# Performance work log

Hardware: AMD Instinct MI355X
Metric: run time of the kernel (lower is better)

## Reference

```python
import jax, jax.numpy as jnp
import numpy as np

ETYPES = ((0, 2), (4, 6))  # per-metapath edge-type indices into the doubled r_vec table
ALPHA = 3.0


def celu3(x):
    return jax.nn.celu(x, alpha=ALPHA)


def cmul(a, b):
    # complex multiply, last dim = (real, imag)
    re = a[..., 0] * b[..., 0] - a[..., 1] * b[..., 1]
    im = a[..., 0] * b[..., 1] + a[..., 1] * b[..., 0]
    return jnp.stack([re, im], axis=-1)


def setup_inputs() -> dict:
    key = jax.random.key(0)
    ks = jax.random.split(key, 10)
    N, H, heads, M, E, P = 50000, 64, 4, 2, 250000, 3
    R, FH = 4, 128
    D = heads * H
    return {
        "features": jax.random.normal(ks[0], (N, H), jnp.float32),
        "r_vec": jax.random.normal(ks[1], (R, H // 2, 2), jnp.float32),
        "attn1_w": jax.random.normal(ks[2], (heads, H), jnp.float32) * 0.1,
        "attn2": jax.random.normal(ks[3], (1, heads, H), jnp.float32) * 0.1,
        "fw1": jax.random.normal(ks[4], (2 * FH, D), jnp.float32) * 0.05,
        "fb1": jnp.zeros((2 * FH,), jnp.float32),
        "fw2": jax.random.normal(ks[5], (FH, 2 * FH), jnp.float32) * 0.05,
        "fb2": jnp.zeros((FH,), jnp.float32),
        "fw3": jax.random.normal(ks[6], (1, FH), jnp.float32) * 0.05,
        "instances": jax.random.randint(ks[7], (M, E, P), 0, N, jnp.int32),
    }


def reference(features, r_vec, attn1_w, attn2, fw1, fb1, fw2, fb2, fw3, instances):
    N, H = features.shape
    M, E, P = instances.shape
    heads = attn1_w.shape[0]
    # unit-modulus rotations + conjugates: [2R, H/2, 2], even=r, odd=conj(r)
    rv = r_vec / jnp.linalg.norm(r_vec, axis=2, keepdims=True)
    conj = rv * jnp.array([1.0, -1.0], rv.dtype)
    rv2 = jnp.stack([rv, conj], axis=1).reshape(-1, H // 2, 2)

    per_path = []
    for m in range(M):
        inst = instances[m]  # [E, P]
        # backward cumulative rotation: final_r[i] = prod_{j>=i} r_{etype[j]}, final_r[P-1]=1
        ident = jnp.stack([jnp.ones(H // 2, rv.dtype), jnp.zeros(H // 2, rv.dtype)], axis=-1)
        frs = [ident]
        for i in range(P - 2, -1, -1):
            frs.insert(0, cmul(frs[0], rv2[ETYPES[m][i]]))
        fr = jnp.stack(frs)  # [P, H/2, 2]
        # gather features along metapath and rotate (last position rotated by identity)
        edata = features[inst].reshape(E, P, H // 2, 2)
        rot = cmul(edata, fr[None])
        me = jnp.mean(rot.reshape(E, P, H), axis=1)  # [E, H]
        se = celu3(me) * jax.nn.sigmoid(me)  # gated metapath embedding
        eft = celu3(se)  # same across heads in original (tiled)
        seg = inst[:, 0]  # target node per instance
        a1 = celu3(features[seg] @ attn1_w.T)  # [E, heads]
        a2 = jnp.einsum('eh,kh->ek', eft, attn2[0])  # [E, heads]
        a = celu3(a1 + a2)
        # segment softmax over each node's instance set
        amax = jax.ops.segment_max(a, seg, num_segments=N)
        ex = jnp.exp(a - amax[seg])
        den = jax.ops.segment_sum(ex, seg, num_segments=N)
        attn = ex / den[seg]  # [E, heads]
        hsum = jax.ops.segment_sum(attn[:, :, None] * eft[:, None, :], seg, num_segments=N)
        per_path.append(celu3(hsum).reshape(N, heads * H))  # empty nodes -> 0

    z = jnp.stack(per_path, axis=1)  # [N, M, D]
    t = celu3(z @ fw1.T + fb1)
    t = celu3(t @ fw2.T + fb2)
    w = (t @ fw3.T).mean(axis=0)  # [M, 1]
    beta = jax.nn.softmax(w, axis=0)
    out = (beta * z).sum(axis=1)  # [N, D]
    return out
```

## Files before the change

kernel.cpp:

```cpp
#include <hip/hip_runtime.h>
#include <hip/hip_bf16.h>

typedef unsigned short u16;
typedef unsigned int   u32;
typedef short bf16x8 __attribute__((ext_vector_type(8)));
typedef float f32x4  __attribute__((ext_vector_type(4)));

#define CAP 64

__device__ inline float b2f(u16 u){ return __builtin_bit_cast(float, (u32)u << 16); }
__device__ inline u16 f2b(float f){
  u32 x = __builtin_bit_cast(u32, f);
  x += 0x7fffu + ((x >> 16) & 1u);
  return (u16)(x >> 16);
}
__device__ inline u32 pk2(float lo, float hi){
  float2 f; f.x = lo; f.y = hi;
  __hip_bfloat162 h = __float22bfloat162_rn(f);
  u32 r; __builtin_memcpy(&r, &h, 4);
  return r;
}
__device__ inline void up2(u32 u, float& lo, float& hi){
  lo = __builtin_bit_cast(float, u << 16);
  hi = __builtin_bit_cast(float, u & 0xffff0000u);
}
__device__ inline float fexp(float x){ return __expf(x); }
__device__ inline float celu3(float x){
  return x > 0.f ? x : 3.f * (__expf(x * (1.f/3.f)) - 1.f);
}
__device__ inline float sigm(float x){ return 1.f / (1.f + __expf(-x)); }

__global__ __launch_bounds__(256) void conv_kernel(
    const float* __restrict__ src, u16* __restrict__ dst, int n8)
{
  int i = blockIdx.x * 256 + threadIdx.x;
  if (i >= n8) return;
  float4 a = ((const float4*)src)[2*i], b = ((const float4*)src)[2*i + 1];
  uint4 o;
  o.x = pk2(a.x, a.y);
  o.y = pk2(a.z, a.w);
  o.z = pk2(b.x, b.y);
  o.w = pk2(b.z, b.w);
  ((uint4*)dst)[i] = o;
}

__global__ __launch_bounds__(256) void a1_kernel(
    const float* __restrict__ feat, const float* __restrict__ attn1,
    u16* __restrict__ featb, float* __restrict__ a1c, int N)
{
  __shared__ float w1s[256];
  int t = threadIdx.x;
  w1s[t] = attn1[t];
  __syncthreads();
  int g = t >> 4, l = t & 15;
  int n = blockIdx.x * 16 + g;
  if (n >= N) return;
  float4 x = ((const float4*)feat)[(size_t)n*16 + l];
  uint2 o;
  o.x = pk2(x.x, x.y);
  o.y = pk2(x.z, x.w);
  ((uint2*)featb)[(size_t)n*16 + l] = o;
  float d[4];
  #pragma unroll
  for (int k = 0; k < 4; ++k){
    int wb = k*64 + l*4;
    d[k] = x.x*w1s[wb] + x.y*w1s[wb+1] + x.z*w1s[wb+2] + x.w*w1s[wb+3];
  }
  #pragma unroll
  for (int off = 8; off; off >>= 1){
    #pragma unroll
    for (int k = 0; k < 4; ++k) d[k] += __shfl_xor(d[k], off);
  }
  if (l == 0){
    float4 av;
    av.x = celu3(d[0]); av.y = celu3(d[1]);
    av.z = celu3(d[2]); av.w = celu3(d[3]);
    ((float4*)a1c)[n] = av;
  }
}

__global__ void fr_kernel(const float* __restrict__ rvec, float* __restrict__ fr){
  int c = threadIdx.x;
  if (c >= 32) return;
  for (int m = 0; m < 2; ++m){
    float ar = rvec[(2*m)*64 + c*2],   ai = rvec[(2*m)*64 + c*2 + 1];
    float br = rvec[(2*m+1)*64 + c*2], bi = rvec[(2*m+1)*64 + c*2 + 1];
    float na = rsqrtf(ar*ar + ai*ai); ar *= na; ai *= na;
    float nb = rsqrtf(br*br + bi*bi); br *= nb; bi *= nb;
    float* f = fr + m*128;
    f[c*2]        = br*ar - bi*ai;
    f[c*2 + 1]    = br*ai + bi*ar;
    f[64 + c*2]   = br;
    f[64 + c*2+1] = bi;
  }
}

__global__ __launch_bounds__(256) void edge_kernel(
    const u16* __restrict__ featb, const int* __restrict__ inst,
    const float* __restrict__ fr, const float* __restrict__ a1c,
    const float* __restrict__ attn2, u16* __restrict__ eft,
    float* __restrict__ a_ws, int* __restrict__ cnt, int* __restrict__ bucket,
    int E, int N)
{
  __shared__ float frs[128];
  __shared__ float w2s[256];
  int m = blockIdx.y;
  int t = threadIdx.x;
  if (t < 128) frs[t] = fr[m*128 + t];
  w2s[t] = attn2[t];
  __syncthreads();

  int g = t >> 4, l = t & 15;
  int e = blockIdx.x * 16 + g;
  if (e >= E) return;
  int base = (m*E + e)*3;
  int i0 = inst[base], i1 = inst[base+1], i2 = inst[base+2];

  const uint2* fb = (const uint2*)featb;
  uint2 v0 = fb[(size_t)i0*16 + l];
  uint2 v1 = fb[(size_t)i1*16 + l];
  uint2 v2 = fb[(size_t)i2*16 + l];
  float f0[4], f1[4], f2v[4];
  up2(v0.x, f0[0], f0[1]); up2(v0.y, f0[2], f0[3]);
  up2(v1.x, f1[0], f1[1]); up2(v1.y, f1[2], f1[3]);
  up2(v2.x, f2v[0], f2v[1]); up2(v2.y, f2v[2], f2v[3]);

  float4 R0 = *(const float4*)&frs[4*l];
  float4 R1 = *(const float4*)&frs[64 + 4*l];

  float mre0 = (f0[0]*R0.x - f0[1]*R0.y + f1[0]*R1.x - f1[1]*R1.y + f2v[0]) * (1.f/3.f);
  float mim0 = (f0[0]*R0.y + f0[1]*R0.x + f1[0]*R1.y + f1[1]*R1.x + f2v[1]) * (1.f/3.f);
  float mre1 = (f0[2]*R0.z - f0[3]*R0.w + f1[2]*R1.z - f1[3]*R1.w + f2v[2]) * (1.f/3.f);
  float mim1 = (f0[2]*R0.w + f0[3]*R0.z + f1[2]*R1.w + f1[3]*R1.z + f2v[3]) * (1.f/3.f);

  float ef[4], s;
  s = celu3(mre0) * sigm(mre0); ef[0] = celu3(s);
  s = celu3(mim0) * sigm(mim0); ef[1] = celu3(s);
  s = celu3(mre1) * sigm(mre1); ef[2] = celu3(s);
  s = celu3(mim1) * sigm(mim1); ef[3] = celu3(s);

  uint2 uo;
  uo.x = pk2(ef[0], ef[1]);
  uo.y = pk2(ef[2], ef[3]);
  ((uint2*)eft)[(size_t)(m*E + e)*16 + l] = uo;

  float d2[4];
  #pragma unroll
  for (int k = 0; k < 4; ++k){
    int wb = k*64 + l*4;
    d2[k] = ef[0]*w2s[wb] + ef[1]*w2s[wb+1] + ef[2]*w2s[wb+2] + ef[3]*w2s[wb+3];
  }
  #pragma unroll
  for (int off = 8; off; off >>= 1){
    #pragma unroll
    for (int k = 0; k < 4; ++k) d2[k] += __shfl_xor(d2[k], off);
  }
  if (l == 0){
    float4 a1v = ((const float4*)a1c)[i0];
    float4 av;
    av.x = celu3(a1v.x + d2[0]);
    av.y = celu3(a1v.y + d2[1]);
    av.z = celu3(a1v.z + d2[2]);
    av.w = celu3(a1v.w + d2[3]);
    ((float4*)a_ws)[m*E + e] = av;
    int pos = atomicAdd(&cnt[m*N + i0], 1);
    if (pos < CAP) bucket[(size_t)(m*N + i0)*CAP + pos] = e;
  }
}

__global__ __launch_bounds__(256) void seg_kernel(
    const float* __restrict__ a_ws, const u16* __restrict__ eft,
    const int* __restrict__ cnt, const int* __restrict__ bucket,
    u16* __restrict__ z, int E, int N)
{
  int m = blockIdx.y;
  int n = blockIdx.x * 4 + (threadIdx.x >> 6);
  if (n >= N) return;
  int lane = threadIdx.x & 63;
  int sidx = m*N + n;
  int deg = cnt[sidx]; if (deg > CAP) deg = CAP;

  float h0=0.f, h1=0.f, h2=0.f, h3=0.f;
  float d0=0.f, d1=0.f, d2=0.f, d3=0.f;
  if (deg > 0){
    const int* bk = bucket + (size_t)sidx * CAP;
    size_t ebase = (size_t)m * E;

    int e = (lane < deg) ? bk[lane] : 0;
    float w0 = 0.f, w1 = 0.f, w2 = 0.f, w3 = 0.f;
    if (lane < deg){
      float4 av = ((const float4*)a_ws)[ebase + e];
      w0 = fexp(av.x); w1 = fexp(av.y); w2 = fexp(av.z); w3 = fexp(av.w);
    }

    const u16* ep = eft + ebase*64;
    for (int j = 0; j < deg; ++j){
      int   ej  = __shfl(e,  j);
      float a0j = __shfl(w0, j), a1j = __shfl(w1, j);
      float a2j = __shfl(w2, j), a3j = __shfl(w3, j);
      float ev = b2f(ep[(size_t)ej*64 + lane]);
      h0 += a0j*ev; h1 += a1j*ev; h2 += a2j*ev; h3 += a3j*ev;
      d0 += a0j;    d1 += a1j;    d2 += a2j;    d3 += a3j;
    }
    h0 /= d0; h1 /= d1; h2 /= d2; h3 /= d3;
  }
  u16* zr = z + (size_t)sidx*256 + lane;
  zr[0]   = f2b(celu3(h0));
  zr[64]  = f2b(celu3(h1));
  zr[128] = f2b(celu3(h2));
  zr[192] = f2b(celu3(h3));
}

__global__ __launch_bounds__(512, 4) void mlp_kernel(
    const u16* __restrict__ z, const u16* __restrict__ fw1b, const float* __restrict__ fb1,
    const u16* __restrict__ fw2b, const float* __restrict__ fb2, const float* __restrict__ fw3,
    float* __restrict__ waccP, int rows, int N)
{
  __shared__ u16 buf[64][264];
  __shared__ float fw3s[128];
  __shared__ float sPart[8][64];
  int tid = threadIdx.x;
  int row0 = blockIdx.x * 64;
  int wv = tid >> 6, lane = tid & 63, lr = lane & 15, quad = lane >> 4;

  const uint4* zg = (const uint4*)z;
  uint4 zr4[4];
  #pragma unroll
  for (int it = 0; it < 4; ++it){
    int idx = it*512 + tid;
    int row = idx >> 5, c8 = idx & 31;
    int gr = row0 + row;
    zr4[it] = make_uint4(0u,0u,0u,0u);
    if (gr < rows) zr4[it] = zg[(size_t)gr*32 + c8];
  }

  const u16* wb1 = fw1b + (size_t)(wv*32 + lr)*256 + quad*8;
  bf16x8 B1[2][8];
  #pragma unroll
  for (int nt = 0; nt < 2; ++nt)
    #pragma unroll
    for (int ks = 0; ks < 8; ++ks)
      B1[nt][ks] = *(const bf16x8*)(wb1 + nt*16*256 + ks*32);

  if (tid < 128) fw3s[tid] = fw3[tid];

  #pragma unroll
  for (int it = 0; it < 4; ++it){
    int idx = it*512 + tid;
    int row = idx >> 5, c8 = idx & 31;
    *(uint4*)&buf[row][c8*8] = zr4[it];
  }
  __syncthreads();

  f32x4 zero4 = {0.f, 0.f, 0.f, 0.f};

  f32x4 acc[4][2];
  #pragma unroll
  for (int a = 0; a < 4; ++a){ acc[a][0] = zero4; acc[a][1] = zero4; }
  #pragma unroll
  for (int ks = 0; ks < 8; ++ks){
    #pragma unroll
    for (int mt = 0; mt < 4; ++mt){
      bf16x8 af = *(const bf16x8*)&buf[mt*16 + lr][ks*32 + quad*8];
      acc[mt][0] = __builtin_amdgcn_mfma_f32_16x16x32_bf16(af, B1[0][ks], acc[mt][0], 0, 0, 0);
      acc[mt][1] = __builtin_amdgcn_mfma_f32_16x16x32_bf16(af, B1[1][ks], acc[mt][1], 0, 0, 0);
    }
  }

  const u16* wb2 = fw2b + (size_t)(wv*16 + lr)*256 + quad*8;
  bf16x8 B2[8];
  #pragma unroll
  for (int ks = 0; ks < 8; ++ks)
    B2[ks] = *(const bf16x8*)(wb2 + ks*32);

  __syncthreads();
  #pragma unroll
  for (int nt = 0; nt < 2; ++nt){
    int col = wv*32 + nt*16 + lr;
    float bias = fb1[col];
    #pragma unroll
    for (int mt = 0; mt < 4; ++mt)
      #pragma unroll
      for (int ri = 0; ri < 4; ++ri){
        int row = mt*16 + quad*4 + ri;
        buf[row][col] = f2b(celu3(acc[mt][nt][ri] + bias));
      }
  }
  __syncthreads();

  f32x4 acc2[4];
  #pragma unroll
  for (int a = 0; a < 4; ++a) acc2[a] = zero4;
  #pragma unroll
  for (int ks = 0; ks < 8; ++ks){
    #pragma unroll
    for (int mt = 0; mt < 4; ++mt){
      bf16x8 af = *(const bf16x8*)&buf[mt*16 + lr][ks*32 + quad*8];
      acc2[mt] = __builtin_amdgcn_mfma_f32_16x16x32_bf16(af, B2[ks], acc2[mt], 0, 0, 0);
    }
  }

  {
    int col = wv*16 + lr;
    float bias2 = fb2[col];
    float w3 = fw3s[col];
    float ps[4][4];
    #pragma unroll
    for (int mt = 0; mt < 4; ++mt)
      #pragma unroll
      for (int ri = 0; ri < 4; ++ri)
        ps[mt][ri] = celu3(acc2[mt][ri] + bias2) * w3;
    #pragma unroll
    for (int off = 8; off; off >>= 1)
      #pragma unroll
      for (int mt = 0; mt < 4; ++mt)
        #pragma unroll
        for (int ri = 0; ri < 4; ++ri)
          ps[mt][ri] += __shfl_xor(ps[mt][ri], off);
    if (lr == 0){
      #pragma unroll
      for (int mt = 0; mt < 4; ++mt)
        #pragma unroll
        for (int ri = 0; ri < 4; ++ri)
          sPart[wv][mt*16 + quad*4 + ri] = ps[mt][ri];
    }
  }
  __syncthreads();

  if (tid < 64){
    float s = 0.f;
    #pragma unroll
    for (int w = 0; w < 8; ++w) s += sPart[w][tid];
    int gr = row0 + tid;
    if (gr >= rows) s = 0.f;
    float s0 = (gr < N) ? s : 0.f;
    float s1 = (gr < N) ? 0.f : s;
    #pragma unroll
    for (int off = 32; off; off >>= 1){
      s0 += __shfl_xor(s0, off);
      s1 += __shfl_xor(s1, off);
    }
    if (tid == 0){
      int slot = blockIdx.x & 63;
      atomicAdd(&waccP[slot],      s0);
      atomicAdd(&waccP[64 + slot], s1);
    }
  }
}

__global__ void beta_kernel(float* __restrict__ wacc, float invN){
  int t = threadIdx.x;
  float s0 = wacc[t], s1 = wacc[64 + t];
  #pragma unroll
  for (int off = 32; off; off >>= 1){
    s0 += __shfl_xor(s0, off);
    s1 += __shfl_xor(s1, off);
  }
  if (t == 0){
    float w0 = s0*invN, w1 = s1*invN;
    float mx = fmaxf(w0, w1);
    float e0 = __expf(w0 - mx), e1 = __expf(w1 - mx);
    float s = e0 + e1;
    wacc[128] = e0 / s;
    wacc[129] = e1 / s;
  }
}

__global__ __launch_bounds__(256) void out_kernel(
    const u16* __restrict__ z, const float* __restrict__ wacc,
    float* __restrict__ out, int total)
{
  int idx = blockIdx.x * 256 + threadIdx.x;
  if (idx*8 >= total) return;
  float b0 = wacc[128], b1 = wacc[129];
  uint4 u0 = ((const uint4*)z)[idx];
  uint4 u1 = ((const uint4*)z)[(total >> 3) + idx];
  float a0,a1v,c0,c1;
  float4 o;
  up2(u0.x, a0, a1v); up2(u1.x, c0, c1);
  o.x = b0*a0 + b1*c0; o.y = b0*a1v + b1*c1;
  up2(u0.y, a0, a1v); up2(u1.y, c0, c1);
  o.z = b0*a0 + b1*c0; o.w = b0*a1v + b1*c1;
  ((float4*)out)[idx*2] = o;
  up2(u0.z, a0, a1v); up2(u1.z, c0, c1);
  o.x = b0*a0 + b1*c0; o.y = b0*a1v + b1*c1;
  up2(u0.w, a0, a1v); up2(u1.w, c0, c1);
  o.z = b0*a0 + b1*c0; o.w = b0*a1v + b1*c1;
  ((float4*)out)[idx*2 + 1] = o;
}

extern "C" void kernel_launch(void* const* d_in, const int* in_sizes, int n_in,
                              void* d_out, int out_size, void* d_ws, size_t ws_size,
                              hipStream_t stream)
{
  (void)n_in; (void)out_size; (void)ws_size;
  const float* feat  = (const float*)d_in[0];
  const float* rvec  = (const float*)d_in[1];
  const float* attn1 = (const float*)d_in[2];
  const float* attn2 = (const float*)d_in[3];
  const float* fw1   = (const float*)d_in[4];
  const float* fb1   = (const float*)d_in[5];
  const float* fw2   = (const float*)d_in[6];
  const float* fb2   = (const float*)d_in[7];
  const float* fw3   = (const float*)d_in[8];
  const int*   inst  = (const int*)d_in[9];

  int N = in_sizes[0] / 64;
  int E = in_sizes[9] / 6;

  char* ws = (char*)d_ws;
  u16*   z      = (u16*)ws;                            size_t zB = (size_t)2*N*256*2;
  u16*   eft    = (u16*)(ws + zB);                     size_t eB = (size_t)2*E*64*2;
  float* a_ws   = (float*)(ws + zB + eB);              size_t aB = (size_t)2*E*4*4;
  int*   bucket = (int*)(ws + zB + eB + aB);           size_t bB = (size_t)2*N*CAP*4;
  int*   cnt    = (int*)(ws + zB + eB + aB + bB);      size_t cB = (size_t)2*N*4;
  u16*   featb  = (u16*)(ws + zB + eB + aB + bB + cB); size_t fB = (size_t)N*64*2;
  float* a1c    = (float*)(ws + zB + eB + aB + bB + cB + fB);  size_t a1B = (size_t)N*4*4;
  u16*   fw1b   = (u16*)(ws + zB + eB + aB + bB + cB + fB + a1B);
  u16*   fw2b   = fw1b + 256*256;
  float* fr     = (float*)(fw2b + 128*256);
  float* wacc   = fr + 256;

  hipMemsetAsync(cnt, 0, cB, stream);
  hipMemsetAsync(wacc, 0, 128*sizeof(float), stream);

  a1_kernel<<<(N + 15)/16, 256, 0, stream>>>(feat, attn1, featb, a1c, N);
  conv_kernel<<<(256*256/8 + 255)/256, 256, 0, stream>>>(fw1, fw1b, 256*256/8);
  conv_kernel<<<(128*256/8 + 255)/256, 256, 0, stream>>>(fw2, fw2b, 128*256/8);
  fr_kernel<<<1, 64, 0, stream>>>(rvec, fr);
  edge_kernel<<<dim3((E + 15)/16, 2), 256, 0, stream>>>(
      featb, inst, fr, a1c, attn2, eft, a_ws, cnt, bucket, E, N);
  seg_kernel<<<dim3((N + 3)/4, 2), 256, 0, stream>>>(a_ws, eft, cnt, bucket, z, E, N);
  mlp_kernel<<<(2*N + 63)/64, 512, 0, stream>>>(z, fw1b, fb1, fw2b, fb2, fw3, wacc, 2*N, N);
  beta_kernel<<<1, 64, 0, stream>>>(wacc, 1.f/(float)N);
  out_kernel<<<((N*256/8) + 255)/256, 256, 0, stream>>>(z, wacc, (float*)d_out, N*256);
}
```

Measured before the change: 285.9 us.

## Pre-rotate node features per metapath, merge prep kernels, and stage segment weights in LDS

Merges the feature conversion, a1 projection, weight conversions and rotation setup into one pre_kernel. That kernel also precomputes the rotated bf16 feature tables for metapath positions 0 and 1, reusing the z buffer, so edge_kernel only gathers and sums. The activation chain is rewritten to share one exp between celu and sigmoid and to use fast reciprocals. seg_kernel stages edge ids and softmax weights in LDS instead of per-iteration shuffles, reduces the denominator with a butterfly, and unrolls the gather by two. The cost is extra writes for the rotated tables, a little bf16 rounding of rotated values, and fewer kernel launches.

```diff
diff --git a/kernel.cpp b/kernel.cpp
--- a/kernel.cpp
+++ b/kernel.cpp
@@ -25,41 +25,72 @@
   hi = __builtin_bit_cast(float, u & 0xffff0000u);
 }
 __device__ inline float fexp(float x){ return __expf(x); }
+__device__ inline float frcp(float x){ return __builtin_amdgcn_rcpf(x); }
 __device__ inline float celu3(float x){
   return x > 0.f ? x : 3.f * (__expf(x * (1.f/3.f)) - 1.f);
 }
-__device__ inline float sigm(float x){ return 1.f / (1.f + __expf(-x)); }
-
-__global__ __launch_bounds__(256) void conv_kernel(
-    const float* __restrict__ src, u16* __restrict__ dst, int n8)
-{
-  int i = blockIdx.x * 256 + threadIdx.x;
-  if (i >= n8) return;
-  float4 a = ((const float4*)src)[2*i], b = ((const float4*)src)[2*i + 1];
-  uint4 o;
-  o.x = pk2(a.x, a.y);
-  o.y = pk2(a.z, a.w);
-  o.z = pk2(b.x, b.y);
-  o.w = pk2(b.z, b.w);
-  ((uint4*)dst)[i] = o;
-}
-
-__global__ __launch_bounds__(256) void a1_kernel(
+__device__ inline float act_chain(float x){
+  float u  = __expf(x * (1.f/3.f));
+  float u3 = u*u*u;
+  float sg = u3 * frcp(u3 + 1.f);
+  float c1 = x > 0.f ? x : 3.f*u - 3.f;
+  float se = c1 * sg;
+  return se > 0.f ? se : 3.f*__expf(se*(1.f/3.f)) - 3.f;
+}
+
+__global__ __launch_bounds__(256) void pre_kernel(
     const float* __restrict__ feat, const float* __restrict__ attn1,
-    u16* __restrict__ featb, float* __restrict__ a1c, int N)
-{
-  __shared__ float w1s[256];
-  int t = threadIdx.x;
+    const float* __restrict__ rvec, const float* __restrict__ fw1,
+    const float* __restrict__ fw2,
+    u16* __restrict__ featb, u16* __restrict__ rotA, u16* __restrict__ rotB,
+    float* __restrict__ a1c, u16* __restrict__ fw1b, u16* __restrict__ fw2b,
+    int N, int nbA)
+{
+  __shared__ float w1s[256], rvs[256];
+  int b = blockIdx.x, t = threadIdx.x;
+  if (b >= nbA){
+    int cb = b - nbA;
+    const float* src = (cb < 32) ? fw1 : fw2;
+    u16* dst = (cb < 32) ? fw1b : fw2b;
+    int i = (cb < 32 ? cb : cb - 32)*256 + t;
+    float4 a = ((const float4*)src)[2*i], bb = ((const float4*)src)[2*i + 1];
+    uint4 o;
+    o.x = pk2(a.x, a.y);  o.y = pk2(a.z, a.w);
+    o.z = pk2(bb.x, bb.y); o.w = pk2(bb.z, bb.w);
+    ((uint4*)dst)[i] = o;
+    return;
+  }
   w1s[t] = attn1[t];
+  rvs[t] = rvec[t];
   __syncthreads();
   int g = t >> 4, l = t & 15;
-  int n = blockIdx.x * 16 + g;
+  int n = b * 16 + g;
   if (n >= N) return;
   float4 x = ((const float4*)feat)[(size_t)n*16 + l];
   uint2 o;
   o.x = pk2(x.x, x.y);
   o.y = pk2(x.z, x.w);
   ((uint2*)featb)[(size_t)n*16 + l] = o;
+
+  #pragma unroll
+  for (int m = 0; m < 2; ++m){
+    float4 ra = *(const float4*)&rvs[(2*m)*64 + l*4];
+    float4 rb = *(const float4*)&rvs[(2*m+1)*64 + l*4];
+    float na0 = rsqrtf(ra.x*ra.x + ra.y*ra.y); ra.x*=na0; ra.y*=na0;
+    float na1 = rsqrtf(ra.z*ra.z + ra.w*ra.w); ra.z*=na1; ra.w*=na1;
+    float nb0 = rsqrtf(rb.x*rb.x + rb.y*rb.y); rb.x*=nb0; rb.y*=nb0;
+    float nb1 = rsqrtf(rb.z*rb.z + rb.w*rb.w); rb.z*=nb1; rb.w*=nb1;
+    float A0r = rb.x*ra.x - rb.y*ra.y, A0i = rb.x*ra.y + rb.y*ra.x;
+    float A1r = rb.z*ra.z - rb.w*ra.w, A1i = rb.z*ra.w + rb.w*ra.z;
+    uint2 oa, ob;
+    oa.x = pk2(x.x*A0r - x.y*A0i, x.x*A0i + x.y*A0r);
+    oa.y = pk2(x.z*A1r - x.w*A1i, x.z*A1i + x.w*A1r);
+    ob.x = pk2(x.x*rb.x - x.y*rb.y, x.x*rb.y + x.y*rb.x);
+    ob.y = pk2(x.z*rb.z - x.w*rb.w, x.z*rb.w + x.w*rb.z);
+    ((uint2*)rotA)[((size_t)m*N + n)*16 + l] = oa;
+    ((uint2*)rotB)[((size_t)m*N + n)*16 + l] = ob;
+  }
+
   float d[4];
   #pragma unroll
   for (int k = 0; k < 4; ++k){
@@ -79,34 +110,16 @@
   }
 }
 
-__global__ void fr_kernel(const float* __restrict__ rvec, float* __restrict__ fr){
-  int c = threadIdx.x;
-  if (c >= 32) return;
-  for (int m = 0; m < 2; ++m){
-    float ar = rvec[(2*m)*64 + c*2],   ai = rvec[(2*m)*64 + c*2 + 1];
-    float br = rvec[(2*m+1)*64 + c*2], bi = rvec[(2*m+1)*64 + c*2 + 1];
-    float na = rsqrtf(ar*ar + ai*ai); ar *= na; ai *= na;
-    float nb = rsqrtf(br*br + bi*bi); br *= nb; bi *= nb;
-    float* f = fr + m*128;
-    f[c*2]        = br*ar - bi*ai;
-    f[c*2 + 1]    = br*ai + bi*ar;
-    f[64 + c*2]   = br;
-    f[64 + c*2+1] = bi;
-  }
-}
-
 __global__ __launch_bounds__(256) void edge_kernel(
+    const u16* __restrict__ rotA, const u16* __restrict__ rotB,
     const u16* __restrict__ featb, const int* __restrict__ inst,
-    const float* __restrict__ fr, const float* __restrict__ a1c,
-    const float* __restrict__ attn2, u16* __restrict__ eft,
-    float* __restrict__ a_ws, int* __restrict__ cnt, int* __restrict__ bucket,
-    int E, int N)
-{
-  __shared__ float frs[128];
+    const float* __restrict__ a1c, const float* __restrict__ attn2,
+    u16* __restrict__ eft, float* __restrict__ a_ws,
+    int* __restrict__ cnt, int* __restrict__ bucket, int E, int N)
+{
   __shared__ float w2s[256];
   int m = blockIdx.y;
   int t = threadIdx.x;
-  if (t < 128) frs[t] = fr[m*128 + t];
   w2s[t] = attn2[t];
   __syncthreads();
 
@@ -115,29 +128,21 @@
   if (e >= E) return;
   int base = (m*E + e)*3;
   int i0 = inst[base], i1 = inst[base+1], i2 = inst[base+2];
-
-  const uint2* fb = (const uint2*)featb;
-  uint2 v0 = fb[(size_t)i0*16 + l];
-  uint2 v1 = fb[(size_t)i1*16 + l];
-  uint2 v2 = fb[(size_t)i2*16 + l];
-  float f0[4], f1[4], f2v[4];
-  up2(v0.x, f0[0], f0[1]); up2(v0.y, f0[2], f0[3]);
-  up2(v1.x, f1[0], f1[1]); up2(v1.y, f1[2], f1[3]);
-  up2(v2.x, f2v[0], f2v[1]); up2(v2.y, f2v[2], f2v[3]);
-
-  float4 R0 = *(const float4*)&frs[4*l];
-  float4 R1 = *(const float4*)&frs[64 + 4*l];
-
-  float mre0 = (f0[0]*R0.x - f0[1]*R0.y + f1[0]*R1.x - f1[1]*R1.y + f2v[0]) * (1.f/3.f);
-  float mim0 = (f0[0]*R0.y + f0[1]*R0.x + f1[0]*R1.y + f1[1]*R1.x + f2v[1]) * (1.f/3.f);
-  float mre1 = (f0[2]*R0.z - f0[3]*R0.w + f1[2]*R1.z - f1[3]*R1.w + f2v[2]) * (1.f/3.f);
-  float mim1 = (f0[2]*R0.w + f0[3]*R0.z + f1[2]*R1.w + f1[3]*R1.z + f2v[3]) * (1.f/3.f);
-
-  float ef[4], s;
-  s = celu3(mre0) * sigm(mre0); ef[0] = celu3(s);
-  s = celu3(mim0) * sigm(mim0); ef[1] = celu3(s);
-  s = celu3(mre1) * sigm(mre1); ef[2] = celu3(s);
-  s = celu3(mim1) * sigm(mim1); ef[3] = celu3(s);
+  size_t mN = (size_t)m * N;
+
+  uint2 v0 = ((const uint2*)rotA)[(mN + i0)*16 + l];
+  uint2 v1 = ((const uint2*)rotB)[(mN + i1)*16 + l];
+  uint2 v2 = ((const uint2*)featb)[(size_t)i2*16 + l];
+  float a0,a1v,a2v,a3, b0,b1,b2,b3, c0,c1,c2,c3;
+  up2(v0.x, a0, a1v); up2(v0.y, a2v, a3);
+  up2(v1.x, b0, b1);  up2(v1.y, b2, b3);
+  up2(v2.x, c0, c1);  up2(v2.y, c2, c3);
+
+  float ef[4];
+  ef[0] = act_chain((a0 + b0 + c0) * (1.f/3.f));
+  ef[1] = act_chain((a1v + b1 + c1) * (1.f/3.f));
+  ef[2] = act_chain((a2v + b2 + c2) * (1.f/3.f));
+  ef[3] = act_chain((a3 + b3 + c3) * (1.f/3.f));
 
   uint2 uo;
   uo.x = pk2(ef[0], ef[1]);
@@ -156,12 +161,12 @@
     for (int k = 0; k < 4; ++k) d2[k] += __shfl_xor(d2[k], off);
   }
   if (l == 0){
-    float4 a1v = ((const float4*)a1c)[i0];
+    float4 a1v4 = ((const float4*)a1c)[i0];
     float4 av;
-    av.x = celu3(a1v.x + d2[0]);
-    av.y = celu3(a1v.y + d2[1]);
-    av.z = celu3(a1v.z + d2[2]);
-    av.w = celu3(a1v.w + d2[3]);
+    av.x = celu3(a1v4.x + d2[0]);
+    av.y = celu3(a1v4.y + d2[1]);
+    av.z = celu3(a1v4.z + d2[2]);
+    av.w = celu3(a1v4.w + d2[3]);
     ((float4*)a_ws)[m*E + e] = av;
     int pos = atomicAdd(&cnt[m*N + i0], 1);
     if (pos < CAP) bucket[(size_t)(m*N + i0)*CAP + pos] = e;
@@ -173,15 +178,17 @@
     const int* __restrict__ cnt, const int* __restrict__ bucket,
     u16* __restrict__ z, int E, int N)
 {
+  __shared__ float wls[4][64][4];
+  __shared__ int   els[4][64];
+  int wvb = threadIdx.x >> 6;
   int m = blockIdx.y;
-  int n = blockIdx.x * 4 + (threadIdx.x >> 6);
+  int n = blockIdx.x * 4 + wvb;
   if (n >= N) return;
   int lane = threadIdx.x & 63;
   int sidx = m*N + n;
   int deg = cnt[sidx]; if (deg > CAP) deg = CAP;
 
   float h0=0.f, h1=0.f, h2=0.f, h3=0.f;
-  float d0=0.f, d1=0.f, d2=0.f, d3=0.f;
   if (deg > 0){
     const int* bk = bucket + (size_t)sidx * CAP;
     size_t ebase = (size_t)m * E;
@@ -192,17 +199,34 @@
       float4 av = ((const float4*)a_ws)[ebase + e];
       w0 = fexp(av.x); w1 = fexp(av.y); w2 = fexp(av.z); w3 = fexp(av.w);
     }
-
-    const u16* ep = eft + ebase*64;
-    for (int j = 0; j < deg; ++j){
-      int   ej  = __shfl(e,  j);
-      float a0j = __shfl(w0, j), a1j = __shfl(w1, j);
-      float a2j = __shfl(w2, j), a3j = __shfl(w3, j);
-      float ev = b2f(ep[(size_t)ej*64 + lane]);
-      h0 += a0j*ev; h1 += a1j*ev; h2 += a2j*ev; h3 += a3j*ev;
-      d0 += a0j;    d1 += a1j;    d2 += a2j;    d3 += a3j;
-    }
-    h0 /= d0; h1 /= d1; h2 /= d2; h3 /= d3;
+    els[wvb][lane] = e;
+    *(float4*)&wls[wvb][lane][0] = make_float4(w0, w1, w2, w3);
+
+    float d0=w0, d1=w1, d2=w2, d3=w3;
+    #pragma unroll
+    for (int off = 32; off; off >>= 1){
+      d0 += __shfl_xor(d0, off); d1 += __shfl_xor(d1, off);
+      d2 += __shfl_xor(d2, off); d3 += __shfl_xor(d3, off);
+    }
+
+    const u16* ep = eft + ebase*64 + lane;
+    int j = 0;
+    for (; j + 1 < deg; j += 2){
+      int ej0 = els[wvb][j], ej1 = els[wvb][j+1];
+      float4 wj0 = *(const float4*)&wls[wvb][j][0];
+      float4 wj1 = *(const float4*)&wls[wvb][j+1][0];
+      float ev0 = b2f(ep[(size_t)ej0*64]);
+      float ev1 = b2f(ep[(size_t)ej1*64]);
+      h0 += wj0.x*ev0; h1 += wj0.y*ev0; h2 += wj0.z*ev0; h3 += wj0.w*ev0;
+      h0 += wj1.x*ev1; h1 += wj1.y*ev1; h2 += wj1.z*ev1; h3 += wj1.w*ev1;
+    }
+    if (j < deg){
+      int ej0 = els[wvb][j];
+      float4 wj0 = *(const float4*)&wls[wvb][j][0];
+      float ev0 = b2f(ep[(size_t)ej0*64]);
+      h0 += wj0.x*ev0; h1 += wj0.y*ev0; h2 += wj0.z*ev0; h3 += wj0.w*ev0;
+    }
+    h0 *= frcp(d0); h1 *= frcp(d1); h2 *= frcp(d2); h3 *= frcp(d3);
   }
   u16* zr = z + (size_t)sidx*256 + lane;
   zr[0]   = f2b(celu3(h0));
@@ -418,18 +442,19 @@
   float* a1c    = (float*)(ws + zB + eB + aB + bB + cB + fB);  size_t a1B = (size_t)N*4*4;
   u16*   fw1b   = (u16*)(ws + zB + eB + aB + bB + cB + fB + a1B);
   u16*   fw2b   = fw1b + 256*256;
-  float* fr     = (float*)(fw2b + 128*256);
-  float* wacc   = fr + 256;
+  float* wacc   = (float*)(fw2b + 128*256);
+
+  u16* rotA = z;
+  u16* rotB = z + (size_t)2*N*64;
 
   hipMemsetAsync(cnt, 0, cB, stream);
   hipMemsetAsync(wacc, 0, 128*sizeof(float), stream);
 
-  a1_kernel<<<(N + 15)/16, 256, 0, stream>>>(feat, attn1, featb, a1c, N);
-  conv_kernel<<<(256*256/8 + 255)/256, 256, 0, stream>>>(fw1, fw1b, 256*256/8);
-  conv_kernel<<<(128*256/8 + 255)/256, 256, 0, stream>>>(fw2, fw2b, 128*256/8);
-  fr_kernel<<<1, 64, 0, stream>>>(rvec, fr);
+  int nbA = (N + 15)/16;
+  pre_kernel<<<nbA + 48, 256, 0, stream>>>(
+      feat, attn1, rvec, fw1, fw2, featb, rotA, rotB, a1c, fw1b, fw2b, N, nbA);
   edge_kernel<<<dim3((E + 15)/16, 2), 256, 0, stream>>>(
-      featb, inst, fr, a1c, attn2, eft, a_ws, cnt, bucket, E, N);
+      rotA, rotB, featb, inst, a1c, attn2, eft, a_ws, cnt, bucket, E, N);
   seg_kernel<<<dim3((N + 3)/4, 2), 256, 0, stream>>>(a_ws, eft, cnt, bucket, z, E, N);
   mlp_kernel<<<(2*N + 63)/64, 512, 0, stream>>>(z, fw1b, fb1, fw2b, fb2, fw3, wacc, 2*N, N);
   beta_kernel<<<1, 64, 0, stream>>>(wacc, 1.f/(float)N);
```

New measurement: 273.6 us. -4.3%, faster.
